# Kernel optimization log

Measured on AMD Instinct MI355X. Metric: run time of the kernel, lower is better.

## Reference

```python
import jax, jax.numpy as jnp
import numpy as np

N = 100000
E = 1600000
IN_C, HID, OUT_C = 128, 128, 64
NUM_LAYERS = 3


def setup_inputs() -> dict:
    key = jax.random.key(0)
    ks = jax.random.split(key, 8)
    x = jax.random.normal(ks[0], (N, IN_C), dtype=jnp.float32)
    edge_index = jax.random.randint(ks[1], (2, E), 0, N, dtype=jnp.int64)
    s_in = 1.0 / np.sqrt(IN_C)
    s_h = 1.0 / np.sqrt(HID)
    W_in = jax.random.uniform(ks[2], (IN_C, HID), jnp.float32, -s_in, s_in)
    b_in = jax.random.uniform(ks[3], (HID,), jnp.float32, -s_in, s_in)
    conv_W = jax.random.uniform(ks[4], (NUM_LAYERS, HID, HID), jnp.float32, -s_h, s_h)
    conv_b = jnp.zeros((NUM_LAYERS, HID), jnp.float32)
    W_out = jax.random.uniform(ks[5], (HID, OUT_C), jnp.float32, -s_h, s_h)
    b_out = jax.random.uniform(ks[6], (OUT_C,), jnp.float32, -s_h, s_h)
    return {"x": x, "edge_index": edge_index, "W_in": W_in, "b_in": b_in,
            "conv_W": conv_W, "conv_b": conv_b, "W_out": W_out, "b_out": b_out}


def reference(x, edge_index, W_in, b_in, conv_W, conv_b, W_out, b_out):
    n = x.shape[0]
    loops = jnp.arange(n, dtype=edge_index.dtype)
    # add self-loops (PyG GCNConv default)
    rows = jnp.concatenate([edge_index[0], loops])  # source nodes
    cols = jnp.concatenate([edge_index[1], loops])  # target nodes
    deg = jax.ops.segment_sum(jnp.ones_like(cols, dtype=x.dtype), cols, num_segments=n)
    dinv = jnp.where(deg > 0, jax.lax.rsqrt(deg), 0.0)
    norm = (dinv[rows] * dinv[cols])[:, None]  # [E+N, 1] symmetric normalization

    def gcn_conv(h, W, b):
        h = h @ W  # [N, HID]
        msg = h[rows] * norm  # gather + scale, [E+N, HID]
        return jax.ops.segment_sum(msg, cols, num_segments=n) + b

    h = jax.nn.relu(x @ W_in + b_in)
    for l in range(conv_W.shape[0]):
        h = jax.nn.relu(gcn_conv(h, conv_W[l], conv_b[l]))
    logits = h @ W_out + b_out
    return logits
```

## Files before the change

kernel.cpp:

```cpp
#include <hip/hip_runtime.h>

typedef __attribute__((ext_vector_type(8))) short short8;
typedef __attribute__((ext_vector_type(4))) float f32x4;

#define NPB   128
#define CAPB  2688
#define TILE  8192
#define MAXB  800

__device__ __forceinline__ float bf2f(unsigned short u){
  union { float f; unsigned u; } v; v.u = ((unsigned)u) << 16; return v.f;
}
__device__ __forceinline__ unsigned short f2bf(float f){
  union { float f; unsigned u; } v; v.f = f;
  unsigned r = v.u + 0x7fffu + ((v.u >> 16) & 1u);
  return (unsigned short)(r >> 16);
}

__global__ void k_detect(const unsigned* ei, int* flag){
  unsigned v = ei[2*threadIdx.x + 1];
  unsigned long long any = __ballot(v != 0u);
  if (threadIdx.x == 0) flag[0] = (any == 0ull) ? 1 : 0;
}

__global__ __launch_bounds__(256) void k_bucket2(const void* ei, const int* __restrict__ flag,
    int* __restrict__ bcnt, unsigned* __restrict__ buf, int E, int nbuck)
{
  __shared__ unsigned recs[TILE];
  __shared__ unsigned short recb[TILE];
  __shared__ int cnt[MAXB];
  __shared__ int offs[MAXB];
  __shared__ int ofc[MAXB];
  __shared__ int gbase[MAXB];
  __shared__ int sc[256];

  const int tid = threadIdx.x;
  const bool i64 = flag[0] != 0;
  const int e0 = blockIdx.x * TILE;
  const int m = min(TILE, E - e0);
  if (m <= 0) return;

  for (int i = tid; i < nbuck; i += 256) cnt[i] = 0;
  __syncthreads();

  for (int i = tid; i < m; i += 256){
    int c = i64 ? (int)((const long long*)ei)[(size_t)E + e0 + i]
                : ((const int*)ei)[(size_t)E + e0 + i];
    atomicAdd(&cnt[c >> 7], 1);
  }
  __syncthreads();

  int lc[4]; int tsum = 0;
#pragma unroll
  for (int j = 0; j < 4; ++j){
    int b = tid*4 + j;
    lc[j] = (b < nbuck) ? cnt[b] : 0;
    tsum += lc[j];
  }
  sc[tid] = tsum; __syncthreads();
  for (int off = 1; off < 256; off <<= 1){
    int a = (tid >= off) ? sc[tid - off] : 0;
    __syncthreads(); sc[tid] += a; __syncthreads();
  }
  int run = sc[tid] - tsum;
#pragma unroll
  for (int j = 0; j < 4; ++j){
    int b = tid*4 + j;
    if (b < nbuck){
      offs[b] = run; ofc[b] = run;
      gbase[b] = lc[j] ? atomicAdd(&bcnt[b*16], lc[j]) : 0;
    }
    run += lc[j];
  }
  __syncthreads();

  for (int i = tid; i < m; i += 256){
    int r, c;
    if (i64){ const long long* p = (const long long*)ei; r = (int)p[e0+i]; c = (int)p[(size_t)E+e0+i]; }
    else    { const int* p = (const int*)ei;            r = p[e0+i];      c = p[(size_t)E+e0+i]; }
    int b = c >> 7;
    int pos = atomicAdd(&ofc[b], 1);
    recs[pos] = ((unsigned)(c & (NPB-1)) << 17) | (unsigned)r;
    recb[pos] = (unsigned short)b;
  }
  __syncthreads();

  for (int i = tid; i < m; i += 256){
    int b = recb[i];
    int dst = gbase[b] + (i - offs[b]);
    if (dst < CAPB) buf[(size_t)b*CAPB + dst] = recs[i];
  }
}

__global__ void k_bscan(const int* __restrict__ bcnt, int* __restrict__ bbase,
                        int* __restrict__ indptr, int nbuck, int N, int E){
  __shared__ int s[1024];
  const int tid = threadIdx.x;
  int v = (tid < nbuck) ? min(bcnt[tid*16], CAPB) : 0;
  s[tid] = v; __syncthreads();
  for (int off = 1; off < 1024; off <<= 1){
    int a = (tid >= off) ? s[tid - off] : 0;
    __syncthreads();
    s[tid] += a;
    __syncthreads();
  }
  if (tid < nbuck) bbase[tid] = s[tid] - v;
  if (tid == 0) indptr[N] = E;
}

__global__ __launch_bounds__(256) void k_csr(const int* __restrict__ bcnt,
    const int* __restrict__ bbase, const unsigned* __restrict__ buf,
    int* __restrict__ indptr, int* __restrict__ srcl, float* __restrict__ dinv, int N){
  __shared__ unsigned recs[CAPB];
  __shared__ int cnt[NPB];
  __shared__ int ex[NPB];
  __shared__ int sc[256];
  const int b = blockIdx.x, tid = threadIdx.x;
  const int m = min(bcnt[b*16], CAPB);
  const int base = bbase[b];

  if (tid < NPB) cnt[tid] = 0;
  __syncthreads();
  for (int i = tid; i < m; i += 256){
    unsigned rec = buf[(size_t)b*CAPB + i];
    recs[i] = rec;
    atomicAdd(&cnt[rec >> 17], 1);
  }
  __syncthreads();
  int v = (tid < NPB) ? cnt[tid] : 0;
  sc[tid] = v; __syncthreads();
  for (int off = 1; off < 256; off <<= 1){
    int a = (tid >= off) ? sc[tid - off] : 0;
    __syncthreads();
    sc[tid] += a;
    __syncthreads();
  }
  if (tid < NPB){
    int excl = sc[tid] - v;
    ex[tid] = excl;
    int g = b*NPB + tid;
    if (g < N){
      indptr[g] = base + excl;
      dinv[g]   = rsqrtf((float)v + 1.0f);
    }
  }
  __syncthreads();
  for (int i = tid; i < m; i += 256){
    unsigned rec = recs[i];
    int pos = base + atomicAdd(&ex[rec >> 17], 1);
    srcl[pos] = (int)(rec & 0x1FFFFu);
  }
}

__global__ void k_wprep_all(const float* __restrict__ W_in, const float* __restrict__ convW,
                            const float* __restrict__ W_out, unsigned short* __restrict__ Bf){
  const int slot = blockIdx.x >> 3;
  const int idx  = (blockIdx.x & 7)*256 + threadIdx.x;
  const float* W; int ncol;
  if (slot == 0){ W = W_in; ncol = 128; }
  else if (slot <= 3){ W = convW + (size_t)(slot-1)*128*128; ncol = 128; }
  else { W = W_out; ncol = 64; }
  const int l = idx & 63, ks = (idx >> 6) & 3, cb = idx >> 8;
  if (cb >= (ncol >> 4)) return;
  const int c  = cb*16 + (l & 15);
  const int k0 = ks*32 + ((l >> 4) << 3);
  unsigned short* o = Bf + (size_t)slot*16384 + (size_t)idx*8;
#pragma unroll
  for (int j = 0; j < 8; ++j) o[j] = f2bf(W[(size_t)(k0 + j)*ncol + c]);
}

template<int NCOL, bool A_F32, bool BIAS, bool RELU, bool SCALE, bool OUT_F32>
__global__ __launch_bounds__(256) void k_mm(const void* __restrict__ Ap,
    const unsigned short* __restrict__ Bf, const float* __restrict__ bias,
    const float* __restrict__ dinv, void* __restrict__ Cp, int nrows)
{
  constexpr int NCB = NCOL/16;
  const int tid = threadIdx.x;
  const int wave = tid >> 6, l = tid & 63;
  const int lr = l & 15, lg = l >> 4;
  const int row0 = blockIdx.x*128 + wave*32;

  f32x4 acc[2][NCB];
#pragma unroll
  for (int i = 0; i < 2; ++i)
#pragma unroll
    for (int j = 0; j < NCB; ++j) acc[i][j] = f32x4{0.f, 0.f, 0.f, 0.f};

  const int r0 = row0 + lr, r1 = row0 + 16 + lr;
  const bool ok0 = r0 < nrows, ok1 = r1 < nrows;

#pragma unroll
  for (int ks = 0; ks < 4; ++ks){
    const int kbase = ks*32 + lg*8;
    short8 a0 = short8{0,0,0,0,0,0,0,0}, a1 = short8{0,0,0,0,0,0,0,0};
    if constexpr (A_F32){
      const float* A = (const float*)Ap;
      if (ok0){
        const float* p = A + (size_t)r0*128 + kbase;
        f32x4 x0 = *(const f32x4*)p, x1 = *(const f32x4*)(p + 4);
#pragma unroll
        for (int j = 0; j < 4; ++j){ a0[j] = (short)f2bf(x0[j]); a0[j+4] = (short)f2bf(x1[j]); }
      }
      if (ok1){
        const float* p = A + (size_t)r1*128 + kbase;
        f32x4 x0 = *(const f32x4*)p, x1 = *(const f32x4*)(p + 4);
#pragma unroll
        for (int j = 0; j < 4; ++j){ a1[j] = (short)f2bf(x0[j]); a1[j+4] = (short)f2bf(x1[j]); }
      }
    } else {
      const unsigned short* A = (const unsigned short*)Ap;
      if (ok0) a0 = *(const short8*)(A + (size_t)r0*128 + kbase);
      if (ok1) a1 = *(const short8*)(A + (size_t)r1*128 + kbase);
    }
#pragma unroll
    for (int cb = 0; cb < NCB; ++cb){
      short8 b = *(const short8*)(Bf + ((size_t)(cb*4 + ks)*64 + l)*8);
      acc[0][cb] = __builtin_amdgcn_mfma_f32_16x16x32_bf16(a0, b, acc[0][cb], 0, 0, 0);
      acc[1][cb] = __builtin_amdgcn_mfma_f32_16x16x32_bf16(a1, b, acc[1][cb], 0, 0, 0);
    }
  }

#pragma unroll
  for (int rb = 0; rb < 2; ++rb){
#pragma unroll
    for (int j = 0; j < 4; ++j){
      const int r = row0 + rb*16 + lg*4 + j;
      if (r >= nrows) continue;
      const float dv = SCALE ? dinv[r] : 1.0f;
#pragma unroll
      for (int cb = 0; cb < NCB; ++cb){
        const int c = cb*16 + lr;
        float v = acc[rb][cb][j];
        if constexpr (BIAS) v += bias[c];
        if constexpr (RELU) v = fmaxf(v, 0.0f);
        if constexpr (SCALE) v *= dv;
        if constexpr (OUT_F32) ((float*)Cp)[(size_t)r*NCOL + c] = v;
        else ((unsigned short*)Cp)[(size_t)r*NCOL + c] = f2bf(v);
      }
    }
  }
}

__global__ __launch_bounds__(256) void k_agg(const unsigned* __restrict__ t,
    const int* __restrict__ indptr, const int* __restrict__ srcl,
    const float* __restrict__ dinv, const float* __restrict__ bias,
    unsigned* __restrict__ hout, int n)
{
  const int node = blockIdx.x*4 + (threadIdx.x >> 6);
  if (node >= n) return;
  const int l = threadIdx.x & 63;

  unsigned v = t[(size_t)node*64 + l];
  float a0 = bf2f((unsigned short)v), a1 = bf2f((unsigned short)(v >> 16));

  int i = indptr[node];
  const int e = indptr[node + 1];
  while (i < e){
    int cnt = e - i; if (cnt > 64) cnt = 64;
    int idx = srcl[min(i + l, e - 1)];
    int j = 0;
    for (; j + 16 <= cnt; j += 16){
      int r[16]; unsigned u[16];
#pragma unroll
      for (int q = 0; q < 16; ++q) r[q] = __shfl(idx, j + q);
#pragma unroll
      for (int q = 0; q < 16; ++q) u[q] = t[(size_t)r[q]*64 + l];
#pragma unroll
      for (int q = 0; q < 16; ++q){
        a0 += bf2f((unsigned short)u[q]);
        a1 += bf2f((unsigned short)(u[q] >> 16));
      }
    }
    for (; j + 8 <= cnt; j += 8){
      int r[8]; unsigned u[8];
#pragma unroll
      for (int q = 0; q < 8; ++q) r[q] = __shfl(idx, j + q);
#pragma unroll
      for (int q = 0; q < 8; ++q) u[q] = t[(size_t)r[q]*64 + l];
#pragma unroll
      for (int q = 0; q < 8; ++q){
        a0 += bf2f((unsigned short)u[q]);
        a1 += bf2f((unsigned short)(u[q] >> 16));
      }
    }
    for (; j + 4 <= cnt; j += 4){
      int r[4]; unsigned u[4];
#pragma unroll
      for (int q = 0; q < 4; ++q) r[q] = __shfl(idx, j + q);
#pragma unroll
      for (int q = 0; q < 4; ++q) u[q] = t[(size_t)r[q]*64 + l];
#pragma unroll
      for (int q = 0; q < 4; ++q){
        a0 += bf2f((unsigned short)u[q]);
        a1 += bf2f((unsigned short)(u[q] >> 16));
      }
    }
    for (; j < cnt; ++j){
      int r0 = __shfl(idx, j);
      unsigned u0 = t[(size_t)r0*64 + l];
      a0 += bf2f((unsigned short)u0);
      a1 += bf2f((unsigned short)(u0 >> 16));
    }
    i += cnt;
  }
  const float d = dinv[node];
  float o0 = fmaxf(fmaf(d, a0, bias[2*l]),     0.0f);
  float o1 = fmaxf(fmaf(d, a1, bias[2*l + 1]), 0.0f);
  hout[(size_t)node*64 + l] = (unsigned)f2bf(o0) | ((unsigned)f2bf(o1) << 16);
}

extern "C" void kernel_launch(void* const* d_in, const int* in_sizes, int n_in,
                              void* d_out, int out_size, void* d_ws, size_t ws_size,
                              hipStream_t stream)
{
  const float* x     = (const float*)d_in[0];
  const void*  ei    = d_in[1];
  const float* W_in  = (const float*)d_in[2];
  const float* b_in  = (const float*)d_in[3];
  const float* convW = (const float*)d_in[4];
  const float* convb = (const float*)d_in[5];
  const float* W_out = (const float*)d_in[6];
  const float* b_out = (const float*)d_in[7];
  float* out = (float*)d_out;

  const int N = in_sizes[0] / 128;
  const int E = in_sizes[1] / 2;
  const int NBUCK = (N + NPB - 1) / NPB;

  char* w = (char*)d_ws;
  auto alloc = [&](size_t b){ char* p = w; w += (b + 255) & ~(size_t)255; return p; };
  unsigned short* h    = (unsigned short*)alloc((size_t)N*128*2);
  unsigned short* t    = (unsigned short*)alloc((size_t)N*128*2);
  unsigned short* Bf   = (unsigned short*)alloc((size_t)5*16384*2);
  float* dinv          = (float*)alloc((size_t)N*4);
  int* indptr          = (int*)alloc((size_t)(N+1)*4);
  int* srcl            = (int*)alloc((size_t)E*4);
  int* bcnt            = (int*)alloc((size_t)NBUCK*64);
  int* bbase           = (int*)alloc((size_t)(NBUCK+1)*4);
  int* flag            = (int*)alloc(256);
  unsigned* bbuf       = (unsigned*)t;

  const int MB = (N + 127) / 128;

  k_detect<<<1, 64, 0, stream>>>((const unsigned*)ei, flag);
  (void)hipMemsetAsync(bcnt, 0, (size_t)NBUCK*64, stream);
  k_wprep_all<<<40, 256, 0, stream>>>(W_in, convW, W_out, Bf);
  k_bucket2<<<(E + TILE - 1)/TILE, 256, 0, stream>>>(ei, flag, bcnt, bbuf, E, NBUCK);
  k_bscan <<<1, 1024, 0, stream>>>(bcnt, bbase, indptr, NBUCK, N, E);
  k_csr   <<<NBUCK, 256, 0, stream>>>(bcnt, bbase, bbuf, indptr, srcl, dinv, N);

  k_mm<128, true, true, true, false, false><<<MB, 256, 0, stream>>>(x, Bf, b_in, nullptr, h, N);

  for (int L = 0; L < 3; ++L){
    k_mm<128, false, false, false, true, false><<<MB, 256, 0, stream>>>(h, Bf + (size_t)(1+L)*16384, nullptr, dinv, t, N);
    k_agg<<<(N + 3)/4, 256, 0, stream>>>((const unsigned*)t, indptr, srcl, dinv,
                                         convb + (size_t)L*128, (unsigned*)h, N);
  }

  k_mm<64, false, true, false, false, true><<<MB, 256, 0, stream>>>(h, Bf + (size_t)4*16384, b_out, nullptr, out, N);
}
```

Measured before the change: 352.0 us.

## Store transformed features in column-blocked layout and split aggregation by column group

The per-layer GEMM now writes its bf16 output as 8 column blocks of 16 features, each stored contiguously across all nodes. The aggregation kernel launches 8x more blocks, each handling one column group: 8 lanes cover the 16 features while 8 edge slots per wave are processed in parallel, then reduced with cross-lane shuffles. The aim is to shrink each gathered slab to a 2 MB column block that fits better in cache, and to raise edge-level parallelism. In exchange it reads each CSR index list 8 times and issues only 32-byte gathers per edge row.

```diff
diff --git a/kernel.cpp b/kernel.cpp
--- a/kernel.cpp
+++ b/kernel.cpp
@@ -169,7 +169,7 @@
   for (int j = 0; j < 8; ++j) o[j] = f2bf(W[(size_t)(k0 + j)*ncol + c]);
 }
 
-template<int NCOL, bool A_F32, bool BIAS, bool RELU, bool SCALE, bool OUT_F32>
+template<int NCOL, bool A_F32, bool BIAS, bool RELU, bool SCALE, bool OUT_F32, bool TBLOCK>
 __global__ __launch_bounds__(256) void k_mm(const void* __restrict__ Ap,
     const unsigned short* __restrict__ Bf, const float* __restrict__ bias,
     const float* __restrict__ dinv, void* __restrict__ Cp, int nrows)
@@ -235,78 +235,70 @@
         if constexpr (RELU) v = fmaxf(v, 0.0f);
         if constexpr (SCALE) v *= dv;
         if constexpr (OUT_F32) ((float*)Cp)[(size_t)r*NCOL + c] = v;
+        else if constexpr (TBLOCK)
+          ((unsigned short*)Cp)[(size_t)cb*nrows*16 + (size_t)r*16 + lr] = f2bf(v);
         else ((unsigned short*)Cp)[(size_t)r*NCOL + c] = f2bf(v);
       }
     }
   }
 }
 
-__global__ __launch_bounds__(256) void k_agg(const unsigned* __restrict__ t,
+__global__ __launch_bounds__(256) void k_agg_b(const unsigned* __restrict__ tb,
     const int* __restrict__ indptr, const int* __restrict__ srcl,
     const float* __restrict__ dinv, const float* __restrict__ bias,
     unsigned* __restrict__ hout, int n)
 {
-  const int node = blockIdx.x*4 + (threadIdx.x >> 6);
+  const int g = blockIdx.x & 7;
+  const int node = (blockIdx.x >> 3)*4 + (threadIdx.x >> 6);
   if (node >= n) return;
   const int l = threadIdx.x & 63;
-
-  unsigned v = t[(size_t)node*64 + l];
-  float a0 = bf2f((unsigned short)v), a1 = bf2f((unsigned short)(v >> 16));
+  const int e8 = l >> 3, d = l & 7;
+  const unsigned* tg = tb + (size_t)g*n*8;
+
+  float a0 = 0.f, a1 = 0.f;
+  if (e8 == 0){
+    unsigned u = tg[(size_t)node*8 + d];
+    a0 = bf2f((unsigned short)u); a1 = bf2f((unsigned short)(u >> 16));
+  }
 
   int i = indptr[node];
   const int e = indptr[node + 1];
-  while (i < e){
-    int cnt = e - i; if (cnt > 64) cnt = 64;
-    int idx = srcl[min(i + l, e - 1)];
-    int j = 0;
-    for (; j + 16 <= cnt; j += 16){
-      int r[16]; unsigned u[16];
-#pragma unroll
-      for (int q = 0; q < 16; ++q) r[q] = __shfl(idx, j + q);
-#pragma unroll
-      for (int q = 0; q < 16; ++q) u[q] = t[(size_t)r[q]*64 + l];
-#pragma unroll
-      for (int q = 0; q < 16; ++q){
-        a0 += bf2f((unsigned short)u[q]);
-        a1 += bf2f((unsigned short)(u[q] >> 16));
-      }
-    }
-    for (; j + 8 <= cnt; j += 8){
-      int r[8]; unsigned u[8];
-#pragma unroll
-      for (int q = 0; q < 8; ++q) r[q] = __shfl(idx, j + q);
-#pragma unroll
-      for (int q = 0; q < 8; ++q) u[q] = t[(size_t)r[q]*64 + l];
-#pragma unroll
-      for (int q = 0; q < 8; ++q){
-        a0 += bf2f((unsigned short)u[q]);
-        a1 += bf2f((unsigned short)(u[q] >> 16));
-      }
-    }
-    for (; j + 4 <= cnt; j += 4){
-      int r[4]; unsigned u[4];
-#pragma unroll
-      for (int q = 0; q < 4; ++q) r[q] = __shfl(idx, j + q);
-#pragma unroll
-      for (int q = 0; q < 4; ++q) u[q] = t[(size_t)r[q]*64 + l];
-#pragma unroll
-      for (int q = 0; q < 4; ++q){
-        a0 += bf2f((unsigned short)u[q]);
-        a1 += bf2f((unsigned short)(u[q] >> 16));
-      }
-    }
-    for (; j < cnt; ++j){
-      int r0 = __shfl(idx, j);
-      unsigned u0 = t[(size_t)r0*64 + l];
+  for (; i + 32 <= e; i += 32){
+    int s0 = srcl[i      + e8], s1 = srcl[i + 8  + e8];
+    int s2 = srcl[i + 16 + e8], s3 = srcl[i + 24 + e8];
+    unsigned u0 = tg[(size_t)s0*8 + d], u1 = tg[(size_t)s1*8 + d];
+    unsigned u2 = tg[(size_t)s2*8 + d], u3 = tg[(size_t)s3*8 + d];
+    a0 += bf2f((unsigned short)u0) + bf2f((unsigned short)u1)
+        + bf2f((unsigned short)u2) + bf2f((unsigned short)u3);
+    a1 += bf2f((unsigned short)(u0 >> 16)) + bf2f((unsigned short)(u1 >> 16))
+        + bf2f((unsigned short)(u2 >> 16)) + bf2f((unsigned short)(u3 >> 16));
+  }
+  for (; i + 16 <= e; i += 16){
+    int s0 = srcl[i + e8], s1 = srcl[i + 8 + e8];
+    unsigned u0 = tg[(size_t)s0*8 + d], u1 = tg[(size_t)s1*8 + d];
+    a0 += bf2f((unsigned short)u0) + bf2f((unsigned short)u1);
+    a1 += bf2f((unsigned short)(u0 >> 16)) + bf2f((unsigned short)(u1 >> 16));
+  }
+  for (; i < e; i += 8){
+    int j = i + e8;
+    if (j < e){
+      int s0 = srcl[j];
+      unsigned u0 = tg[(size_t)s0*8 + d];
       a0 += bf2f((unsigned short)u0);
       a1 += bf2f((unsigned short)(u0 >> 16));
     }
-    i += cnt;
-  }
-  const float d = dinv[node];
-  float o0 = fmaxf(fmaf(d, a0, bias[2*l]),     0.0f);
-  float o1 = fmaxf(fmaf(d, a1, bias[2*l + 1]), 0.0f);
-  hout[(size_t)node*64 + l] = (unsigned)f2bf(o0) | ((unsigned)f2bf(o1) << 16);
+  }
+
+  a0 += __shfl_xor(a0, 8);  a1 += __shfl_xor(a1, 8);
+  a0 += __shfl_xor(a0, 16); a1 += __shfl_xor(a1, 16);
+  a0 += __shfl_xor(a0, 32); a1 += __shfl_xor(a1, 32);
+
+  if (e8 == 0){
+    const float dv = dinv[node];
+    float o0 = fmaxf(fmaf(dv, a0, bias[g*16 + 2*d]),     0.0f);
+    float o1 = fmaxf(fmaf(dv, a1, bias[g*16 + 2*d + 1]), 0.0f);
+    hout[(size_t)node*64 + g*8 + d] = (unsigned)f2bf(o0) | ((unsigned)f2bf(o1) << 16);
+  }
 }
 
 extern "C" void kernel_launch(void* const* d_in, const int* in_sizes, int n_in,
@@ -349,13 +341,13 @@
   k_bscan <<<1, 1024, 0, stream>>>(bcnt, bbase, indptr, NBUCK, N, E);
   k_csr   <<<NBUCK, 256, 0, stream>>>(bcnt, bbase, bbuf, indptr, srcl, dinv, N);
 
-  k_mm<128, true, true, true, false, false><<<MB, 256, 0, stream>>>(x, Bf, b_in, nullptr, h, N);
+  k_mm<128, true, true, true, false, false, false><<<MB, 256, 0, stream>>>(x, Bf, b_in, nullptr, h, N);
 
   for (int L = 0; L < 3; ++L){
-    k_mm<128, false, false, false, true, false><<<MB, 256, 0, stream>>>(h, Bf + (size_t)(1+L)*16384, nullptr, dinv, t, N);
-    k_agg<<<(N + 3)/4, 256, 0, stream>>>((const unsigned*)t, indptr, srcl, dinv,
-                                         convb + (size_t)L*128, (unsigned*)h, N);
-  }
-
-  k_mm<64, false, true, false, false, true><<<MB, 256, 0, stream>>>(h, Bf + (size_t)4*16384, b_out, nullptr, out, N);
-}
+    k_mm<128, false, false, false, true, false, true><<<MB, 256, 0, stream>>>(h, Bf + (size_t)(1+L)*16384, nullptr, dinv, t, N);
+    k_agg_b<<<8*((N + 3)/4), 256, 0, stream>>>((const unsigned*)t, indptr, srcl, dinv,
+                                               convb + (size_t)L*128, (unsigned*)h, N);
+  }
+
+  k_mm<64, false, true, false, false, true, false><<<MB, 256, 0, stream>>>(h, Bf + (size_t)4*16384, b_out, nullptr, out, N);
+}
```

Result: slower. 895.9 us (+154.5%).

## Merge preprocessing launches and prefetch neighbor indices in aggregation

Applied to the files above, without the earlier changes.

Cuts the CSR build from six stream operations to three. Index-width detection moves into the bucketing kernel, zeroing of bucket counters moves into the weight-prep kernel, and the separate scan kernel is dropped. Each CSR block now claims its base offset with an atomic cursor, so nodes store (start, count) spans instead of a prefix-sum indptr. The aggregation kernel prefetches the next chunk of source indices, uses readlane instead of shuffle, and takes an occupancy hint; the atomic cursor makes bucket order in srcl nondeterministic but keeps it correct.

```diff
diff --git a/kernel.cpp b/kernel.cpp
--- a/kernel.cpp
+++ b/kernel.cpp
@@ -8,8 +8,11 @@
 #define TILE  8192
 #define MAXB  800
 
-__device__ __forceinline__ float bf2f(unsigned short u){
-  union { float f; unsigned u; } v; v.u = ((unsigned)u) << 16; return v.f;
+__device__ __forceinline__ float bfLO(unsigned u){
+  union { unsigned x; float f; } c; c.x = u << 16; return c.f;
+}
+__device__ __forceinline__ float bfHI(unsigned u){
+  union { unsigned x; float f; } c; c.x = u & 0xffff0000u; return c.f;
 }
 __device__ __forceinline__ unsigned short f2bf(float f){
   union { float f; unsigned u; } v; v.f = f;
@@ -17,143 +20,14 @@
   return (unsigned short)(r >> 16);
 }
 
-__global__ void k_detect(const unsigned* ei, int* flag){
-  unsigned v = ei[2*threadIdx.x + 1];
-  unsigned long long any = __ballot(v != 0u);
-  if (threadIdx.x == 0) flag[0] = (any == 0ull) ? 1 : 0;
-}
-
-__global__ __launch_bounds__(256) void k_bucket2(const void* ei, const int* __restrict__ flag,
-    int* __restrict__ bcnt, unsigned* __restrict__ buf, int E, int nbuck)
-{
-  __shared__ unsigned recs[TILE];
-  __shared__ unsigned short recb[TILE];
-  __shared__ int cnt[MAXB];
-  __shared__ int offs[MAXB];
-  __shared__ int ofc[MAXB];
-  __shared__ int gbase[MAXB];
-  __shared__ int sc[256];
-
-  const int tid = threadIdx.x;
-  const bool i64 = flag[0] != 0;
-  const int e0 = blockIdx.x * TILE;
-  const int m = min(TILE, E - e0);
-  if (m <= 0) return;
-
-  for (int i = tid; i < nbuck; i += 256) cnt[i] = 0;
-  __syncthreads();
-
-  for (int i = tid; i < m; i += 256){
-    int c = i64 ? (int)((const long long*)ei)[(size_t)E + e0 + i]
-                : ((const int*)ei)[(size_t)E + e0 + i];
-    atomicAdd(&cnt[c >> 7], 1);
-  }
-  __syncthreads();
-
-  int lc[4]; int tsum = 0;
-#pragma unroll
-  for (int j = 0; j < 4; ++j){
-    int b = tid*4 + j;
-    lc[j] = (b < nbuck) ? cnt[b] : 0;
-    tsum += lc[j];
-  }
-  sc[tid] = tsum; __syncthreads();
-  for (int off = 1; off < 256; off <<= 1){
-    int a = (tid >= off) ? sc[tid - off] : 0;
-    __syncthreads(); sc[tid] += a; __syncthreads();
-  }
-  int run = sc[tid] - tsum;
-#pragma unroll
-  for (int j = 0; j < 4; ++j){
-    int b = tid*4 + j;
-    if (b < nbuck){
-      offs[b] = run; ofc[b] = run;
-      gbase[b] = lc[j] ? atomicAdd(&bcnt[b*16], lc[j]) : 0;
-    }
-    run += lc[j];
-  }
-  __syncthreads();
-
-  for (int i = tid; i < m; i += 256){
-    int r, c;
-    if (i64){ const long long* p = (const long long*)ei; r = (int)p[e0+i]; c = (int)p[(size_t)E+e0+i]; }
-    else    { const int* p = (const int*)ei;            r = p[e0+i];      c = p[(size_t)E+e0+i]; }
-    int b = c >> 7;
-    int pos = atomicAdd(&ofc[b], 1);
-    recs[pos] = ((unsigned)(c & (NPB-1)) << 17) | (unsigned)r;
-    recb[pos] = (unsigned short)b;
-  }
-  __syncthreads();
-
-  for (int i = tid; i < m; i += 256){
-    int b = recb[i];
-    int dst = gbase[b] + (i - offs[b]);
-    if (dst < CAPB) buf[(size_t)b*CAPB + dst] = recs[i];
-  }
-}
-
-__global__ void k_bscan(const int* __restrict__ bcnt, int* __restrict__ bbase,
-                        int* __restrict__ indptr, int nbuck, int N, int E){
-  __shared__ int s[1024];
-  const int tid = threadIdx.x;
-  int v = (tid < nbuck) ? min(bcnt[tid*16], CAPB) : 0;
-  s[tid] = v; __syncthreads();
-  for (int off = 1; off < 1024; off <<= 1){
-    int a = (tid >= off) ? s[tid - off] : 0;
-    __syncthreads();
-    s[tid] += a;
-    __syncthreads();
-  }
-  if (tid < nbuck) bbase[tid] = s[tid] - v;
-  if (tid == 0) indptr[N] = E;
-}
-
-__global__ __launch_bounds__(256) void k_csr(const int* __restrict__ bcnt,
-    const int* __restrict__ bbase, const unsigned* __restrict__ buf,
-    int* __restrict__ indptr, int* __restrict__ srcl, float* __restrict__ dinv, int N){
-  __shared__ unsigned recs[CAPB];
-  __shared__ int cnt[NPB];
-  __shared__ int ex[NPB];
-  __shared__ int sc[256];
-  const int b = blockIdx.x, tid = threadIdx.x;
-  const int m = min(bcnt[b*16], CAPB);
-  const int base = bbase[b];
-
-  if (tid < NPB) cnt[tid] = 0;
-  __syncthreads();
-  for (int i = tid; i < m; i += 256){
-    unsigned rec = buf[(size_t)b*CAPB + i];
-    recs[i] = rec;
-    atomicAdd(&cnt[rec >> 17], 1);
-  }
-  __syncthreads();
-  int v = (tid < NPB) ? cnt[tid] : 0;
-  sc[tid] = v; __syncthreads();
-  for (int off = 1; off < 256; off <<= 1){
-    int a = (tid >= off) ? sc[tid - off] : 0;
-    __syncthreads();
-    sc[tid] += a;
-    __syncthreads();
-  }
-  if (tid < NPB){
-    int excl = sc[tid] - v;
-    ex[tid] = excl;
-    int g = b*NPB + tid;
-    if (g < N){
-      indptr[g] = base + excl;
-      dinv[g]   = rsqrtf((float)v + 1.0f);
-    }
-  }
-  __syncthreads();
-  for (int i = tid; i < m; i += 256){
-    unsigned rec = recs[i];
-    int pos = base + atomicAdd(&ex[rec >> 17], 1);
-    srcl[pos] = (int)(rec & 0x1FFFFu);
-  }
-}
-
 __global__ void k_wprep_all(const float* __restrict__ W_in, const float* __restrict__ convW,
-                            const float* __restrict__ W_out, unsigned short* __restrict__ Bf){
+                            const float* __restrict__ W_out, unsigned short* __restrict__ Bf,
+                            int* __restrict__ zeroPtr, int zeroN){
+  if (blockIdx.x >= 40){
+    int i = (blockIdx.x - 40)*256 + threadIdx.x;
+    if (i < zeroN) zeroPtr[i] = 0;
+    return;
+  }
   const int slot = blockIdx.x >> 3;
   const int idx  = (blockIdx.x & 7)*256 + threadIdx.x;
   const float* W; int ncol;
@@ -169,6 +43,127 @@
   for (int j = 0; j < 8; ++j) o[j] = f2bf(W[(size_t)(k0 + j)*ncol + c]);
 }
 
+__global__ __launch_bounds__(256) void k_bucket2(const void* ei,
+    int* __restrict__ bcnt, unsigned* __restrict__ buf, int E, int nbuck)
+{
+  __shared__ unsigned recs[TILE];
+  __shared__ unsigned short recb[TILE];
+  __shared__ int cnt[MAXB];
+  __shared__ int offs[MAXB];
+  __shared__ int ofc[MAXB];
+  __shared__ int gbase[MAXB];
+  __shared__ int sc[256];
+  __shared__ int s_i64;
+
+  const int tid = threadIdx.x;
+  if (tid < 64){
+    unsigned v = ((const unsigned*)ei)[2*tid + 1];
+    unsigned long long any = __ballot(v != 0u);
+    if (tid == 0) s_i64 = (any == 0ull) ? 1 : 0;
+  }
+  const int e0 = blockIdx.x * TILE;
+  const int m = min(TILE, E - e0);
+  if (m <= 0) return;
+
+  for (int i = tid; i < nbuck; i += 256) cnt[i] = 0;
+  __syncthreads();
+  const bool i64 = s_i64 != 0;
+
+  for (int i = tid; i < m; i += 256){
+    int c = i64 ? (int)((const long long*)ei)[(size_t)E + e0 + i]
+                : ((const int*)ei)[(size_t)E + e0 + i];
+    atomicAdd(&cnt[c >> 7], 1);
+  }
+  __syncthreads();
+
+  int lc[4]; int tsum = 0;
+#pragma unroll
+  for (int j = 0; j < 4; ++j){
+    int b = tid*4 + j;
+    lc[j] = (b < nbuck) ? cnt[b] : 0;
+    tsum += lc[j];
+  }
+  sc[tid] = tsum; __syncthreads();
+  for (int off = 1; off < 256; off <<= 1){
+    int a = (tid >= off) ? sc[tid - off] : 0;
+    __syncthreads(); sc[tid] += a; __syncthreads();
+  }
+  int run = sc[tid] - tsum;
+#pragma unroll
+  for (int j = 0; j < 4; ++j){
+    int b = tid*4 + j;
+    if (b < nbuck){
+      offs[b] = run; ofc[b] = run;
+      gbase[b] = lc[j] ? atomicAdd(&bcnt[b*16], lc[j]) : 0;
+    }
+    run += lc[j];
+  }
+  __syncthreads();
+
+  for (int i = tid; i < m; i += 256){
+    int r, c;
+    if (i64){ const long long* p = (const long long*)ei; r = (int)p[e0+i]; c = (int)p[(size_t)E+e0+i]; }
+    else    { const int* p = (const int*)ei;            r = p[e0+i];      c = p[(size_t)E+e0+i]; }
+    int b = c >> 7;
+    int pos = atomicAdd(&ofc[b], 1);
+    recs[pos] = ((unsigned)(c & (NPB-1)) << 17) | (unsigned)r;
+    recb[pos] = (unsigned short)b;
+  }
+  __syncthreads();
+
+  for (int i = tid; i < m; i += 256){
+    int b = recb[i];
+    int dst = gbase[b] + (i - offs[b]);
+    if (dst < CAPB) buf[(size_t)b*CAPB + dst] = recs[i];
+  }
+}
+
+__global__ __launch_bounds__(256) void k_csr2(const int* __restrict__ bcnt,
+    const unsigned* __restrict__ buf, int2* __restrict__ nspan,
+    int* __restrict__ srcl, float* __restrict__ dinv, int* __restrict__ cursor, int N){
+  __shared__ unsigned recs[CAPB];
+  __shared__ int cnt[NPB];
+  __shared__ int ex[NPB];
+  __shared__ int sc[256];
+  __shared__ int s_base;
+  const int b = blockIdx.x, tid = threadIdx.x;
+  const int m = min(bcnt[b*16], CAPB);
+  if (tid == 0) s_base = atomicAdd(cursor, m);
+
+  if (tid < NPB) cnt[tid] = 0;
+  __syncthreads();
+  for (int i = tid; i < m; i += 256){
+    unsigned rec = buf[(size_t)b*CAPB + i];
+    recs[i] = rec;
+    atomicAdd(&cnt[rec >> 17], 1);
+  }
+  __syncthreads();
+  const int base = s_base;
+  int v = (tid < NPB) ? cnt[tid] : 0;
+  sc[tid] = v; __syncthreads();
+  for (int off = 1; off < 256; off <<= 1){
+    int a = (tid >= off) ? sc[tid - off] : 0;
+    __syncthreads();
+    sc[tid] += a;
+    __syncthreads();
+  }
+  if (tid < NPB){
+    int excl = sc[tid] - v;
+    ex[tid] = excl;
+    int g = b*NPB + tid;
+    if (g < N){
+      nspan[g] = make_int2(base + excl, v);
+      dinv[g]  = rsqrtf((float)v + 1.0f);
+    }
+  }
+  __syncthreads();
+  for (int i = tid; i < m; i += 256){
+    unsigned rec = recs[i];
+    int pos = base + atomicAdd(&ex[rec >> 17], 1);
+    srcl[pos] = (int)(rec & 0x1FFFFu);
+  }
+}
+
 template<int NCOL, bool A_F32, bool BIAS, bool RELU, bool SCALE, bool OUT_F32>
 __global__ __launch_bounds__(256) void k_mm(const void* __restrict__ Ap,
     const unsigned short* __restrict__ Bf, const float* __restrict__ bias,
@@ -241,8 +236,8 @@
   }
 }
 
-__global__ __launch_bounds__(256) void k_agg(const unsigned* __restrict__ t,
-    const int* __restrict__ indptr, const int* __restrict__ srcl,
+__global__ __launch_bounds__(256, 8) void k_agg(const unsigned* __restrict__ t,
+    const int2* __restrict__ nspan, const int* __restrict__ srcl,
     const float* __restrict__ dinv, const float* __restrict__ bias,
     unsigned* __restrict__ hout, int n)
 {
@@ -250,58 +245,55 @@
   if (node >= n) return;
   const int l = threadIdx.x & 63;
 
+  const int2 sp = nspan[node];
+  int i = sp.x;
+  const int e = sp.x + sp.y;
+
   unsigned v = t[(size_t)node*64 + l];
-  float a0 = bf2f((unsigned short)v), a1 = bf2f((unsigned short)(v >> 16));
-
-  int i = indptr[node];
-  const int e = indptr[node + 1];
+  float a0 = bfLO(v), a1 = bfHI(v);
+
+  int idx = (i < e) ? srcl[min(i + l, e - 1)] : 0;
   while (i < e){
-    int cnt = e - i; if (cnt > 64) cnt = 64;
-    int idx = srcl[min(i + l, e - 1)];
+    const int cnt = min(e - i, 64);
+    const int nexti = i + cnt;
+    const int idxn = (nexti < e) ? srcl[min(nexti + l, e - 1)] : 0;
     int j = 0;
     for (; j + 16 <= cnt; j += 16){
-      int r[16]; unsigned u[16];
-#pragma unroll
-      for (int q = 0; q < 16; ++q) r[q] = __shfl(idx, j + q);
-#pragma unroll
-      for (int q = 0; q < 16; ++q) u[q] = t[(size_t)r[q]*64 + l];
+      unsigned u[16];
 #pragma unroll
       for (int q = 0; q < 16; ++q){
-        a0 += bf2f((unsigned short)u[q]);
-        a1 += bf2f((unsigned short)(u[q] >> 16));
-      }
+        int s = __builtin_amdgcn_readlane(idx, j + q);
+        u[q] = t[(size_t)s*64 + l];
+      }
+#pragma unroll
+      for (int q = 0; q < 16; ++q){ a0 += bfLO(u[q]); a1 += bfHI(u[q]); }
     }
     for (; j + 8 <= cnt; j += 8){
-      int r[8]; unsigned u[8];
-#pragma unroll
-      for (int q = 0; q < 8; ++q) r[q] = __shfl(idx, j + q);
-#pragma unroll
-      for (int q = 0; q < 8; ++q) u[q] = t[(size_t)r[q]*64 + l];
+      unsigned u[8];
 #pragma unroll
       for (int q = 0; q < 8; ++q){
-        a0 += bf2f((unsigned short)u[q]);
-        a1 += bf2f((unsigned short)(u[q] >> 16));
-      }
+        int s = __builtin_amdgcn_readlane(idx, j + q);
+        u[q] = t[(size_t)s*64 + l];
+      }
+#pragma unroll
+      for (int q = 0; q < 8; ++q){ a0 += bfLO(u[q]); a1 += bfHI(u[q]); }
     }
     for (; j + 4 <= cnt; j += 4){
-      int r[4]; unsigned u[4];
-#pragma unroll
-      for (int q = 0; q < 4; ++q) r[q] = __shfl(idx, j + q);
-#pragma unroll
-      for (int q = 0; q < 4; ++q) u[q] = t[(size_t)r[q]*64 + l];
+      unsigned u[4];
 #pragma unroll
       for (int q = 0; q < 4; ++q){
-        a0 += bf2f((unsigned short)u[q]);
-        a1 += bf2f((unsigned short)(u[q] >> 16));
-      }
+        int s = __builtin_amdgcn_readlane(idx, j + q);
+        u[q] = t[(size_t)s*64 + l];
+      }
+#pragma unroll
+      for (int q = 0; q < 4; ++q){ a0 += bfLO(u[q]); a1 += bfHI(u[q]); }
     }
     for (; j < cnt; ++j){
-      int r0 = __shfl(idx, j);
-      unsigned u0 = t[(size_t)r0*64 + l];
-      a0 += bf2f((unsigned short)u0);
-      a1 += bf2f((unsigned short)(u0 >> 16));
-    }
-    i += cnt;
+      int s = __builtin_amdgcn_readlane(idx, j);
+      unsigned u0 = t[(size_t)s*64 + l];
+      a0 += bfLO(u0); a1 += bfHI(u0);
+    }
+    i = nexti; idx = idxn;
   }
   const float d = dinv[node];
   float o0 = fmaxf(fmaf(d, a0, bias[2*l]),     0.0f);
@@ -333,27 +325,25 @@
   unsigned short* t    = (unsigned short*)alloc((size_t)N*128*2);
   unsigned short* Bf   = (unsigned short*)alloc((size_t)5*16384*2);
   float* dinv          = (float*)alloc((size_t)N*4);
-  int* indptr          = (int*)alloc((size_t)(N+1)*4);
+  int2* nspan          = (int2*)alloc((size_t)N*8);
   int* srcl            = (int*)alloc((size_t)E*4);
-  int* bcnt            = (int*)alloc((size_t)NBUCK*64);
-  int* bbase           = (int*)alloc((size_t)(NBUCK+1)*4);
-  int* flag            = (int*)alloc(256);
+  int* bcnt            = (int*)alloc((size_t)(NBUCK*16 + 16)*4);
   unsigned* bbuf       = (unsigned*)t;
 
+  int* cursor = bcnt + NBUCK*16;
+  const int zeroN = NBUCK*16 + 16;
+  const int ZB = (zeroN + 255)/256;
   const int MB = (N + 127) / 128;
 
-  k_detect<<<1, 64, 0, stream>>>((const unsigned*)ei, flag);
-  (void)hipMemsetAsync(bcnt, 0, (size_t)NBUCK*64, stream);
-  k_wprep_all<<<40, 256, 0, stream>>>(W_in, convW, W_out, Bf);
-  k_bucket2<<<(E + TILE - 1)/TILE, 256, 0, stream>>>(ei, flag, bcnt, bbuf, E, NBUCK);
-  k_bscan <<<1, 1024, 0, stream>>>(bcnt, bbase, indptr, NBUCK, N, E);
-  k_csr   <<<NBUCK, 256, 0, stream>>>(bcnt, bbase, bbuf, indptr, srcl, dinv, N);
+  k_wprep_all<<<40 + ZB, 256, 0, stream>>>(W_in, convW, W_out, Bf, bcnt, zeroN);
+  k_bucket2<<<(E + TILE - 1)/TILE, 256, 0, stream>>>(ei, bcnt, bbuf, E, NBUCK);
+  k_csr2  <<<NBUCK, 256, 0, stream>>>(bcnt, bbuf, nspan, srcl, dinv, cursor, N);
 
   k_mm<128, true, true, true, false, false><<<MB, 256, 0, stream>>>(x, Bf, b_in, nullptr, h, N);
 
   for (int L = 0; L < 3; ++L){
     k_mm<128, false, false, false, true, false><<<MB, 256, 0, stream>>>(h, Bf + (size_t)(1+L)*16384, nullptr, dinv, t, N);
-    k_agg<<<(N + 3)/4, 256, 0, stream>>>((const unsigned*)t, indptr, srcl, dinv,
+    k_agg<<<(N + 3)/4, 256, 0, stream>>>((const unsigned*)t, nspan, srcl, dinv,
                                          convb + (size_t)L*128, (unsigned*)h, N);
   }
 
```

New measurement: 345.3 us. Within noise of the previous version (-1.9%).
